# Kernel tuning notes

Measured on AMD Instinct MI355X. Metric: run time of the kernel, lower is better.

The kernel has to match this reference:

```python
import jax, jax.numpy as jnp
import numpy as np


def setup_inputs() -> dict:
    key = jax.random.key(0)
    ks = jax.random.split(key, 8)
    B, C, H, W = 4, 512, 64, 64
    Cq = C // 8
    s = 1.0 / np.sqrt(C)
    return {
        "x": jax.random.normal(ks[0], (B, C, H, W), jnp.float32),
        "Wq": jax.random.normal(ks[1], (Cq, C), jnp.float32) * s,
        "bq": jax.random.normal(ks[2], (Cq,), jnp.float32) * 0.01,
        "Wk": jax.random.normal(ks[3], (Cq, C), jnp.float32) * s,
        "bk": jax.random.normal(ks[4], (Cq,), jnp.float32) * 0.01,
        "Wv": jax.random.normal(ks[5], (C, C), jnp.float32) * s,
        "bv": jax.random.normal(ks[6], (C,), jnp.float32) * 0.01,
        "gamma": jax.random.normal(ks[7], (1,), jnp.float32),
    }


def reference(x, Wq, bq, Wk, bk, Wv, bv, gamma):
    B, C, H, W = x.shape
    N = H * W
    xf = x.reshape(B, C, N)  # flatten spatial; 1x1 conv == channel matmul
    q = jnp.einsum('oc,bcn->bon', Wq, xf) + bq[None, :, None]  # [B, C/8, N]
    k = jnp.einsum('oc,bcn->bon', Wk, xf) + bk[None, :, None]  # [B, C/8, N]
    v = jnp.einsum('oc,bcn->bon', Wv, xf) + bv[None, :, None]  # [B, C, N]
    energy = jnp.einsum('bdi,bdj->bij', q, k)                  # [B, N, N] (no scaling, as original)
    attention = jax.nn.softmax(energy, axis=-1)
    out = jnp.einsum('bcj,bij->bci', v, attention)             # bmm(v, att^T)
    out = out.reshape(B, C, H, W)
    return gamma[0] * out + x
```

## Files before the change

kernel.cpp:

```cpp
#include <hip/hip_runtime.h>


typedef float    f32x2 __attribute__((ext_vector_type(2)));
typedef float    f32x4 __attribute__((ext_vector_type(4)));
typedef _Float16 f16x4 __attribute__((ext_vector_type(4)));
typedef _Float16 f16x8 __attribute__((ext_vector_type(8)));
typedef short    bf16x8 __attribute__((ext_vector_type(8)));
typedef unsigned short u16x8 __attribute__((ext_vector_type(8)));

#define MFMA_F16(a, b, c)  __builtin_amdgcn_mfma_f32_16x16x32_f16((a), (b), (c), 0, 0, 0)
#define MFMA_BF16(a, b, c) __builtin_amdgcn_mfma_f32_16x16x32_bf16((a), (b), (c), 0, 0, 0)

__device__ __forceinline__ unsigned short bf16_rne(float f) {
    unsigned u = __builtin_bit_cast(unsigned, f);
    u += 0x7FFFu + ((u >> 16) & 1u);
    return (unsigned short)(u >> 16);
}
__device__ __forceinline__ float bf16_f(unsigned short h) {
    unsigned u = (unsigned)h << 16;
    return __builtin_bit_cast(float, u);
}

__device__ __forceinline__ void gload_lds16(const void* g, void* l) {
    __builtin_amdgcn_global_load_lds(
        (const __attribute__((address_space(1))) unsigned int*)g,
        (__attribute__((address_space(3))) unsigned int*)l, 16, 0, 0);
}

#define BARRIER_LGKM() do {                                   \
    asm volatile("s_waitcnt lgkmcnt(0)" ::: "memory");        \
    __builtin_amdgcn_s_barrier();                             \
    asm volatile("" ::: "memory");                            \
} while (0)

#define VM_WAIT8() do {                                       \
    asm volatile("s_waitcnt vmcnt(8)" ::: "memory");          \
    __builtin_amdgcn_sched_barrier(0);                        \
} while (0)
#define VM_WAIT0() do {                                       \
    asm volatile("s_waitcnt vmcnt(0)" ::: "memory");          \
    __builtin_amdgcn_sched_barrier(0);                        \
} while (0)

constexpr int BB = 4, CCH = 512, NS = 4096;

__global__ void prep_kernel(
    const float* __restrict__ Wq, const float* __restrict__ Wk,
    const float* __restrict__ Wv,
    _Float16* __restrict__ Wqh, _Float16* __restrict__ Wkh,
    _Float16* __restrict__ Wvh)
{
    const int idx = blockIdx.x * 256 + threadIdx.x;
    {
        f32x4 v = *(const f32x4*)&Wv[(size_t)idx * 4];
        f16x4 o;
#pragma unroll
        for (int e = 0; e < 4; ++e) o[e] = (_Float16)v[e];
        *(f16x4*)&Wvh[(size_t)idx * 4] = o;
    }
    if (idx < 8192) {
        f32x4 q = *(const f32x4*)&Wq[(size_t)idx * 4];
        f32x4 k = *(const f32x4*)&Wk[(size_t)idx * 4];
        f16x4 qo, ko;
#pragma unroll
        for (int e = 0; e < 4; ++e) { qo[e] = (_Float16)q[e]; ko[e] = (_Float16)k[e]; }
        *(f16x4*)&Wqh[(size_t)idx * 4] = qo;
        *(f16x4*)&Wkh[(size_t)idx * 4] = ko;
    }
}

__global__ __launch_bounds__(512, 4) void proj_kernel(
    const float* __restrict__ x,
    const _Float16* __restrict__ Wqh, const _Float16* __restrict__ Wkh,
    const _Float16* __restrict__ Wvh,
    const float* __restrict__ bq, const float* __restrict__ bk,
    const float* __restrict__ bv,
    _Float16* __restrict__ qws, _Float16* __restrict__ kws,
    unsigned short* __restrict__ vws)
{
    const int t = threadIdx.x, lane = t & 63, w = t >> 6;
    const int l15 = lane & 15, l4 = lane >> 4;
    const int b  = blockIdx.x >> 7;
    const int n0 = (blockIdx.x & 127) * 32;
    const float* xb = x + (size_t)b * CCH * NS;

    __shared__ _Float16 xt[2][32][64];

    f32x4 accv[4][2];
    f32x4 accq[2];
#pragma unroll
    for (int a = 0; a < 4; ++a)
#pragma unroll
        for (int n = 0; n < 2; ++n)
#pragma unroll
            for (int r = 0; r < 4; ++r) accv[a][n][r] = 0.f;
#pragma unroll
    for (int n = 0; n < 2; ++n)
#pragma unroll
        for (int r = 0; r < 4; ++r) accq[n][r] = 0.f;

    const _Float16* Wh = (w < 4) ? Wqh : Wkh;
    const int oq0 = (w & 3) * 16;
    const int stg_c = t >> 3;
    const int stg_n = (t & 7) * 4;

#define PROJ_STAGE(B) do {                                                     \
    char* xb_ = (char*)xt + (B) * 4096;                                        \
    _Pragma("unroll")                                                          \
    for (int u = 0; u < 4; ++u) {                                              \
        const int row = stg_n + u;                                             \
        const int g = ((stg_c >> 3) ^ (row & 7) ^ (((row >> 3) & 3) << 1)) & 7;\
        *(_Float16*)(xb_ + row * 128 + (g << 4) + (stg_c & 7) * 2)             \
            = (_Float16)xv[u];                                                 \
    }                                                                          \
} while (0)

    f32x4 xv = *(const f32x4*)&xb[(size_t)stg_c * NS + n0 + stg_n];
    PROJ_STAGE(0);
    xv = *(const f32x4*)&xb[(size_t)(64 + stg_c) * NS + n0 + stg_n];
    BARRIER_LGKM();

    for (int cc = 0; cc < 8; ++cc) {
        const int buf = cc & 1;
        f16x8 bh[2][2];
#pragma unroll
        for (int nf = 0; nf < 2; ++nf)
#pragma unroll
            for (int ds = 0; ds < 2; ++ds) {
                const int row = nf * 16 + l15;
                const int g = ((ds * 4 + l4) ^ (row & 7) ^ (((row >> 3) & 3) << 1)) & 7;
                bh[nf][ds] = *(const f16x8*)((char*)xt + buf * 4096 + row * 128 + (g << 4));
            }
        PROJ_STAGE(buf ^ 1);
        xv = *(const f32x4*)&xb[(size_t)((((cc + 2) & 7) * 64) + stg_c) * NS + n0 + stg_n];

#pragma unroll
        for (int ds = 0; ds < 2; ++ds) {
            const int c8 = cc * 64 + ds * 32 + l4 * 8;
            f16x8 ahq = *(const f16x8*)&Wh[(size_t)(oq0 + l15) * CCH + c8];
#pragma unroll
            for (int af = 0; af < 4; ++af) {
                f16x8 ah = *(const f16x8*)&Wvh[(size_t)(w * 64 + af * 16 + l15) * CCH + c8];
#pragma unroll
                for (int nf = 0; nf < 2; ++nf)
                    accv[af][nf] = MFMA_F16(ah, bh[nf][ds], accv[af][nf]);
            }
#pragma unroll
            for (int nf = 0; nf < 2; ++nf)
                accq[nf] = MFMA_F16(ahq, bh[nf][ds], accq[nf]);
        }
        BARRIER_LGKM();
    }
#undef PROJ_STAGE

#pragma unroll
    for (int af = 0; af < 4; ++af) {
#pragma unroll
        for (int r = 0; r < 4; ++r) {
            const int o = w * 64 + af * 16 + l4 * 4 + r;
            const float bias = bv[o];
#pragma unroll
            for (int nf = 0; nf < 2; ++nf) {
                const int n = n0 + nf * 16 + l15;
                vws[(size_t)(b * CCH + o) * NS + n] = bf16_rne(accv[af][nf][r] + bias);
            }
        }
    }
    {
        _Float16* oT = (w < 4) ? qws : kws;
        const float* bqk = (w < 4) ? bq : bk;
        float bias[4];
#pragma unroll
        for (int r = 0; r < 4; ++r) bias[r] = bqk[oq0 + l4 * 4 + r];
#pragma unroll
        for (int nf = 0; nf < 2; ++nf) {
            const int n = n0 + nf * 16 + l15;
            f16x4 hv;
#pragma unroll
            for (int r = 0; r < 4; ++r) hv[r] = (_Float16)(accq[nf][r] + bias[r]);
            *(f16x4*)&oT[((size_t)(b * NS + n)) * 64 + oq0 + l4 * 4] = hv;
        }
    }
}

__global__ __launch_bounds__(256, 4) void qk_kernel(
    const _Float16* __restrict__ qws, const _Float16* __restrict__ kws,
    unsigned short* __restrict__ Pws, float* __restrict__ lws2, int b0)
{
    const int t = threadIdx.x, lane = t & 63, w = t >> 6;
    const int l15 = lane & 15, l4 = lane >> 4;
    const int pb = blockIdx.x >> 8;
    const int b  = b0 + pb;
    const int r255 = blockIdx.x & 255;
    const int i0 = (r255 >> 1) * 32;
    const int jh = r255 & 1;
    const int jw = jh * 2048 + w * 512;

    __shared__ unsigned short Pt[4][32][32];
    __shared__ float Lred[4][32];

    f16x8 qa[2][2];
#pragma unroll
    for (int f = 0; f < 2; ++f)
#pragma unroll
        for (int ds = 0; ds < 2; ++ds)
            qa[f][ds] = *(const f16x8*)&qws[((size_t)(b * NS + i0 + f * 16 + l15)) * 64 + ds * 32 + l4 * 8];

    const _Float16* kb = kws + (size_t)b * NS * 64;
    f16x8 kf[2][2];
#pragma unroll
    for (int jf = 0; jf < 2; ++jf)
#pragma unroll
        for (int ds = 0; ds < 2; ++ds)
            kf[jf][ds] = *(const f16x8*)&kb[(size_t)(jw + jf * 16 + l15) * 64 + ds * 32 + l4 * 8];

    f32x4 lacc[2];
#pragma unroll
    for (int f = 0; f < 2; ++f)
#pragma unroll
        for (int r = 0; r < 4; ++r) lacc[f][r] = 0.f;

    char* wbase = (char*)&Pt[w][0][0];
    const int rrow = lane >> 1, h = lane & 1;
    const int rsw = (rrow & 3) ^ (((rrow >> 2) & 1) << 1);
    const int rg0 = (((2 * h)     ^ rsw) & 3) << 4;
    const int rg1 = (((2 * h + 1) ^ rsw) & 3) << 4;
    unsigned short* Pg = Pws + ((size_t)pb * NS + i0 + rrow) * NS + jw + h * 16;

    for (int jt = 0; jt < 16; ++jt) {
        f32x4 e[2][2];
#pragma unroll
        for (int f = 0; f < 2; ++f)
#pragma unroll
            for (int jf = 0; jf < 2; ++jf)
#pragma unroll
                for (int r = 0; r < 4; ++r) e[f][jf][r] = 0.f;
#pragma unroll
        for (int ds = 0; ds < 2; ++ds)
#pragma unroll
            for (int f = 0; f < 2; ++f)
#pragma unroll
                for (int jf = 0; jf < 2; ++jf)
                    e[f][jf] = MFMA_F16(qa[f][ds], kf[jf][ds], e[f][jf]);

        const int jn = jw + ((jt + 1) & 15) * 32;
#pragma unroll
        for (int jf = 0; jf < 2; ++jf)
#pragma unroll
            for (int ds = 0; ds < 2; ++ds)
                kf[jf][ds] = *(const f16x8*)&kb[(size_t)(jn + jf * 16 + l15) * 64 + ds * 32 + l4 * 8];

#pragma unroll
        for (int f = 0; f < 2; ++f)
#pragma unroll
            for (int jf = 0; jf < 2; ++jf) {
                const int col = jf * 16 + l15;
                const int cg = col >> 3;
#pragma unroll
                for (int r = 0; r < 4; ++r) {
                    const int row = f * 16 + l4 * 4 + r;
                    const unsigned short us = bf16_rne(__expf(e[f][jf][r]));
                    lacc[f][r] += bf16_f(us);
                    const int g = ((cg ^ (row & 3) ^ (((row >> 2) & 1) << 1)) & 3) << 4;
                    *(unsigned short*)(wbase + row * 64 + g + (col & 7) * 2) = us;
                }
            }

        asm volatile("s_waitcnt lgkmcnt(0)" ::: "memory");
        __builtin_amdgcn_sched_barrier(0);

        {
            u16x8 va = *(const u16x8*)(wbase + rrow * 64 + rg0);
            u16x8 vb = *(const u16x8*)(wbase + rrow * 64 + rg1);
            *(u16x8*)&Pg[jt * 32]     = va;
            *(u16x8*)&Pg[jt * 32 + 8] = vb;
        }
    }

#pragma unroll
    for (int f = 0; f < 2; ++f)
#pragma unroll
        for (int r = 0; r < 4; ++r) {
            float v = lacc[f][r];
            v += __shfl_xor(v, 1);
            v += __shfl_xor(v, 2);
            v += __shfl_xor(v, 4);
            v += __shfl_xor(v, 8);
            if (l15 == 0) Lred[w][f * 16 + l4 * 4 + r] = v;
        }
    __syncthreads();
    if (t < 32) {
        const float s = Lred[0][t] + Lred[1][t] + Lred[2][t] + Lred[3][t];
        lws2[((size_t)jh * BB + b) * NS + i0 + t] = s;
    }
}

__global__ __launch_bounds__(256, 2) void pv_kernel(
    const unsigned short* __restrict__ Pws, const unsigned short* __restrict__ vws,
    const float* __restrict__ lws2, const float* __restrict__ x,
    const float* __restrict__ gamma, float* __restrict__ out, int b0, int cpx)
{
    const int t = threadIdx.x, lane = t & 63, w = t >> 6;
    const int l15 = lane & 15, l4 = lane >> 4;
    const int bid = (int)blockIdx.x;
    const int swzid = (bid & 7) * cpx + (bid >> 3);
    const int pb = swzid >> 7;
    const int b  = b0 + pb;
    const int r7 = swzid & 127;
    const int in = r7 >> 2, cm = r7 & 3;
    const int wr = w >> 1, wc = w & 1;

    __shared__ unsigned short Vt[2][128][64];
    __shared__ unsigned short Pt2[2][128][64];

    const int srow = w * 8 + (lane >> 3);
    const int sg   = (lane & 7) ^ (srow & 7);
    const unsigned short* gV = vws + ((size_t)(b * CCH + cm * 128 + srow)) * NS + sg * 8;
    const unsigned short* gP = Pws + ((size_t)(pb * NS + in * 128 + srow)) * NS + sg * 8;

    f32x4 acc[4][4];
#pragma unroll
    for (int m = 0; m < 4; ++m)
#pragma unroll
        for (int n = 0; n < 4; ++n)
#pragma unroll
            for (int r = 0; r < 4; ++r) acc[m][n][r] = 0.f;

    int offa[2][4], offb[2][4];
#pragma unroll
    for (int kk = 0; kk < 2; ++kk) {
        const int g = (kk * 4 + l4) ^ (l15 & 7);
#pragma unroll
        for (int m = 0; m < 4; ++m) {
            offa[kk][m] = (wr * 64 + m * 16 + l15) * 128 + g * 16;
            offb[kk][m] = (wc * 64 + m * 16 + l15) * 128 + g * 16;
        }
    }

#define PV_STAGE(kt, buf) do {                                                  \
    const unsigned short* _gV = gV + (size_t)(kt) * 64;                         \
    const unsigned short* _gP = gP + (size_t)(kt) * 64;                         \
    char* _lV = (char*)&Vt[buf][0][0]  + w * 1024;                              \
    char* _lP = (char*)&Pt2[buf][0][0] + w * 1024;                              \
    _Pragma("unroll")                                                           \
    for (int q = 0; q < 4; ++q) {                                               \
        gload_lds16(_gV + (size_t)q * 32 * NS, _lV + q * 4096);                 \
        gload_lds16(_gP + (size_t)q * 32 * NS, _lP + q * 4096);                 \
    }                                                                           \
} while (0)

#define PV_COMPUTE(buf) do {                                                    \
    __builtin_amdgcn_s_setprio(1);                                              \
    _Pragma("unroll")                                                           \
    for (int kk = 0; kk < 2; ++kk) {                                            \
        bf16x8 a[4], bfr[4];                                                    \
        _Pragma("unroll")                                                       \
        for (int m = 0; m < 4; ++m) {                                           \
            a[m]   = *(const bf16x8*)((char*)&Vt[buf][0][0]  + offa[kk][m]);    \
            bfr[m] = *(const bf16x8*)((char*)&Pt2[buf][0][0] + offb[kk][m]);    \
        }                                                                       \
        _Pragma("unroll")                                                       \
        for (int m = 0; m < 4; ++m)                                             \
            _Pragma("unroll")                                                   \
            for (int n = 0; n < 4; ++n)                                         \
                acc[m][n] = MFMA_BF16(a[m], bfr[n], acc[m][n]);                 \
    }                                                                           \
    __builtin_amdgcn_s_setprio(0);                                              \
} while (0)

    PV_STAGE(0, 0);
    for (int kt = 0; kt < 62; kt += 2) {
        PV_STAGE(kt + 1, 1);
        VM_WAIT8();
        __builtin_amdgcn_s_barrier();
        PV_COMPUTE(0);
        BARRIER_LGKM();
        PV_STAGE(kt + 2, 0);
        VM_WAIT8();
        __builtin_amdgcn_s_barrier();
        PV_COMPUTE(1);
        BARRIER_LGKM();
    }
    PV_STAGE(63, 1);
    VM_WAIT8();
    __builtin_amdgcn_s_barrier();
    PV_COMPUTE(0);
    BARRIER_LGKM();
    VM_WAIT0();
    __builtin_amdgcn_s_barrier();
    PV_COMPUTE(1);

#undef PV_STAGE
#undef PV_COMPUTE

    const float gm = gamma[0];
    float linv[4];
#pragma unroll
    for (int n = 0; n < 4; ++n) {
        const int i = in * 128 + wc * 64 + n * 16 + l15;
        linv[n] = 1.f / (lws2[(size_t)b * NS + i] +
                         lws2[((size_t)BB + b) * NS + i]);
    }
#pragma unroll
    for (int m = 0; m < 4; ++m) {
#pragma unroll
        for (int r = 0; r < 4; ++r) {
            const int c = cm * 128 + wr * 64 + m * 16 + l4 * 4 + r;
            const float* xr = x + ((size_t)(b * CCH + c)) * NS;
            float* orow = out + ((size_t)(b * CCH + c)) * NS;
#pragma unroll
            for (int n = 0; n < 4; ++n) {
                const int i = in * 128 + wc * 64 + n * 16 + l15;
                orow[i] = gm * acc[m][n][r] * linv[n] + xr[i];
            }
        }
    }
}

extern "C" void kernel_launch(void* const* d_in, const int* in_sizes, int n_in,
                              void* d_out, int out_size, void* d_ws, size_t ws_size,
                              hipStream_t stream)
{
    const float* x     = (const float*)d_in[0];
    const float* Wq    = (const float*)d_in[1];
    const float* bq    = (const float*)d_in[2];
    const float* Wk    = (const float*)d_in[3];
    const float* bk    = (const float*)d_in[4];
    const float* Wv    = (const float*)d_in[5];
    const float* bv    = (const float*)d_in[6];
    const float* gamma = (const float*)d_in[7];
    float* out = (float*)d_out;

    char* p = (char*)d_ws;
    size_t off = 0;
    auto take = [&](size_t bytes) { char* r = p + off; off += (bytes + 255) & ~(size_t)255; return r; };
    _Float16* qws       = (_Float16*)take((size_t)BB * NS * 64 * 2);
    _Float16* kws       = (_Float16*)take((size_t)BB * NS * 64 * 2);
    unsigned short* vws = (unsigned short*)take((size_t)BB * CCH * NS * 2);
    _Float16* Wvh       = (_Float16*)take((size_t)CCH * CCH * 2);
    _Float16* Wqh       = (_Float16*)take((size_t)64 * CCH * 2);
    _Float16* Wkh       = (_Float16*)take((size_t)64 * CCH * 2);
    float* lws2         = (float*)take((size_t)2 * BB * NS * 4);
    unsigned short* Pws = (unsigned short*)(p + off);

    const size_t P_PER_B = (size_t)NS * NS * 2;
    size_t avail = (ws_size > off) ? (ws_size - off) : 0;
    int nb = (int)(avail / P_PER_B);
    if (nb >= 4) nb = 4; else if (nb >= 2) nb = 2; else nb = 1;

    prep_kernel<<<256, 256, 0, stream>>>(Wq, Wk, Wv, Wqh, Wkh, Wvh);
    proj_kernel<<<512, 512, 0, stream>>>(x, Wqh, Wkh, Wvh, bq, bk, bv,
                                         qws, kws, vws);
    for (int b0 = 0; b0 < BB; b0 += nb) {
        const int nbb = (b0 + nb <= BB) ? nb : (BB - b0);
        qk_kernel<<<nbb * 256, 256, 0, stream>>>(qws, kws, Pws, lws2, b0);
        pv_kernel<<<nbb * 128, 256, 0, stream>>>(Pws, vws, lws2, x, gamma, out,
                                                 b0, (nbb * 128) >> 3);
    }
}
```

Baseline: 167.9 us.

## Enlarge PV tile to 128x256 per block with 8-column MFMA fragments per wave

The PV kernel's output tile grows from 128 channels x 128 positions to 128 x 256 positions. Each wave now holds a 4x8 accumulator array, and the grid shrinks from 128 to 64 blocks per batch. The P staging buffer doubles and the load pattern and vmcnt wait are adjusted to match. This is meant to raise arithmetic intensity and cut redundant V loads from HBM. The cost is more registers, with launch bounds lowered to one block per SIMD, and fewer blocks (256 total) to spread across the CUs.

```diff
diff --git a/kernel.cpp b/kernel.cpp
--- a/kernel.cpp
+++ b/kernel.cpp
@@ -33,8 +33,8 @@
     asm volatile("" ::: "memory");                            \
 } while (0)
 
-#define VM_WAIT8() do {                                       \
-    asm volatile("s_waitcnt vmcnt(8)" ::: "memory");          \
+#define VM_WAIT12() do {                                      \
+    asm volatile("s_waitcnt vmcnt(12)" ::: "memory");         \
     __builtin_amdgcn_sched_barrier(0);                        \
 } while (0)
 #define VM_WAIT0() do {                                       \
@@ -295,7 +295,7 @@
     }
 }
 
-__global__ __launch_bounds__(256, 2) void pv_kernel(
+__global__ __launch_bounds__(256, 1) void pv_kernel(
     const unsigned short* __restrict__ Pws, const unsigned short* __restrict__ vws,
     const float* __restrict__ lws2, const float* __restrict__ x,
     const float* __restrict__ gamma, float* __restrict__ out, int b0, int cpx)
@@ -304,66 +304,69 @@
     const int l15 = lane & 15, l4 = lane >> 4;
     const int bid = (int)blockIdx.x;
     const int swzid = (bid & 7) * cpx + (bid >> 3);
-    const int pb = swzid >> 7;
+    const int pb = swzid >> 6;
     const int b  = b0 + pb;
-    const int r7 = swzid & 127;
-    const int in = r7 >> 2, cm = r7 & 3;
+    const int r6 = swzid & 63;
+    const int in = r6 >> 2, cm = r6 & 3;
     const int wr = w >> 1, wc = w & 1;
 
     __shared__ unsigned short Vt[2][128][64];
-    __shared__ unsigned short Pt2[2][128][64];
-
-    const int srow = w * 8 + (lane >> 3);
-    const int sg   = (lane & 7) ^ (srow & 7);
-    const unsigned short* gV = vws + ((size_t)(b * CCH + cm * 128 + srow)) * NS + sg * 8;
-    const unsigned short* gP = Pws + ((size_t)(pb * NS + in * 128 + srow)) * NS + sg * 8;
-
-    f32x4 acc[4][4];
+    __shared__ unsigned short Pt2[2][256][64];
+
+    const int lrow = lane >> 3;
+    const int sg   = (lane & 7) ^ lrow;
+    const unsigned short* gV = vws + ((size_t)(b * CCH + cm * 128 + w * 32 + lrow)) * NS + sg * 8;
+    const unsigned short* gP = Pws + ((size_t)pb * NS + in * 256 + w * 64 + lrow) * NS + sg * 8;
+
+    f32x4 acc[4][8];
 #pragma unroll
     for (int m = 0; m < 4; ++m)
 #pragma unroll
-        for (int n = 0; n < 4; ++n)
+        for (int n = 0; n < 8; ++n)
 #pragma unroll
             for (int r = 0; r < 4; ++r) acc[m][n][r] = 0.f;
 
-    int offa[2][4], offb[2][4];
+    int offa[2][4], offb[2][8];
 #pragma unroll
     for (int kk = 0; kk < 2; ++kk) {
         const int g = (kk * 4 + l4) ^ (l15 & 7);
 #pragma unroll
-        for (int m = 0; m < 4; ++m) {
+        for (int m = 0; m < 4; ++m)
             offa[kk][m] = (wr * 64 + m * 16 + l15) * 128 + g * 16;
-            offb[kk][m] = (wc * 64 + m * 16 + l15) * 128 + g * 16;
-        }
+#pragma unroll
+        for (int n = 0; n < 8; ++n)
+            offb[kk][n] = (wc * 128 + n * 16 + l15) * 128 + g * 16;
     }
 
 #define PV_STAGE(kt, buf) do {                                                  \
     const unsigned short* _gV = gV + (size_t)(kt) * 64;                         \
     const unsigned short* _gP = gP + (size_t)(kt) * 64;                         \
-    char* _lV = (char*)&Vt[buf][0][0]  + w * 1024;                              \
-    char* _lP = (char*)&Pt2[buf][0][0] + w * 1024;                              \
+    char* _lV = (char*)&Vt[buf][0][0]  + w * 4096;       \
+    char* _lP = (char*)&Pt2[buf][0][0] + w * 8192;       \
     _Pragma("unroll")                                                           \
-    for (int q = 0; q < 4; ++q) {                                               \
-        gload_lds16(_gV + (size_t)q * 32 * NS, _lV + q * 4096);                 \
-        gload_lds16(_gP + (size_t)q * 32 * NS, _lP + q * 4096);                 \
-    }                                                                           \
+    for (int q = 0; q < 4; ++q)                                                 \
+        gload_lds16(_gV + (size_t)q * 8 * NS, _lV + q * 1024);                  \
+    _Pragma("unroll")                                                           \
+    for (int q = 0; q < 8; ++q)                                                 \
+        gload_lds16(_gP + (size_t)q * 8 * NS, _lP + q * 1024);                  \
 } while (0)
 
 #define PV_COMPUTE(buf) do {                                                    \
     __builtin_amdgcn_s_setprio(1);                                              \
     _Pragma("unroll")                                                           \
     for (int kk = 0; kk < 2; ++kk) {                                            \
-        bf16x8 a[4], bfr[4];                                                    \
+        bf16x8 a[4], bb[8];                                                     \
         _Pragma("unroll")                                                       \
-        for (int m = 0; m < 4; ++m) {                                           \
-            a[m]   = *(const bf16x8*)((char*)&Vt[buf][0][0]  + offa[kk][m]);    \
-            bfr[m] = *(const bf16x8*)((char*)&Pt2[buf][0][0] + offb[kk][m]);    \
-        }                                                                       \
+        for (int m = 0; m < 4; ++m)                                             \
+            a[m] = *(const bf16x8*)((char*)&Vt[buf][0][0] + offa[kk][m]);       \
+        _Pragma("unroll")                                                       \
+        for (int n = 0; n < 8; ++n)                                             \
+            bb[n] = *(const bf16x8*)((char*)&Pt2[buf][0][0] + offb[kk][n]);     \
         _Pragma("unroll")                                                       \
         for (int m = 0; m < 4; ++m)                                             \
             _Pragma("unroll")                                                   \
-            for (int n = 0; n < 4; ++n)                                         \
-                acc[m][n] = MFMA_BF16(a[m], bfr[n], acc[m][n]);                 \
+            for (int n = 0; n < 8; ++n)                                         \
+                acc[m][n] = MFMA_BF16(a[m], bb[n], acc[m][n]);                  \
     }                                                                           \
     __builtin_amdgcn_s_setprio(0);                                              \
 } while (0)
@@ -371,18 +374,18 @@
     PV_STAGE(0, 0);
     for (int kt = 0; kt < 62; kt += 2) {
         PV_STAGE(kt + 1, 1);
-        VM_WAIT8();
+        VM_WAIT12();
         __builtin_amdgcn_s_barrier();
         PV_COMPUTE(0);
         BARRIER_LGKM();
         PV_STAGE(kt + 2, 0);
-        VM_WAIT8();
+        VM_WAIT12();
         __builtin_amdgcn_s_barrier();
         PV_COMPUTE(1);
         BARRIER_LGKM();
     }
     PV_STAGE(63, 1);
-    VM_WAIT8();
+    VM_WAIT12();
     __builtin_amdgcn_s_barrier();
     PV_COMPUTE(0);
     BARRIER_LGKM();
@@ -394,10 +397,10 @@
 #undef PV_COMPUTE
 
     const float gm = gamma[0];
-    float linv[4];
-#pragma unroll
-    for (int n = 0; n < 4; ++n) {
-        const int i = in * 128 + wc * 64 + n * 16 + l15;
+    float linv[8];
+#pragma unroll
+    for (int n = 0; n < 8; ++n) {
+        const int i = in * 256 + wc * 128 + n * 16 + l15;
         linv[n] = 1.f / (lws2[(size_t)b * NS + i] +
                          lws2[((size_t)BB + b) * NS + i]);
     }
@@ -409,8 +412,8 @@
             const float* xr = x + ((size_t)(b * CCH + c)) * NS;
             float* orow = out + ((size_t)(b * CCH + c)) * NS;
 #pragma unroll
-            for (int n = 0; n < 4; ++n) {
-                const int i = in * 128 + wc * 64 + n * 16 + l15;
+            for (int n = 0; n < 8; ++n) {
+                const int i = in * 256 + wc * 128 + n * 16 + l15;
                 orow[i] = gm * acc[m][n][r] * linv[n] + xr[i];
             }
         }
@@ -454,7 +457,7 @@
     for (int b0 = 0; b0 < BB; b0 += nb) {
         const int nbb = (b0 + nb <= BB) ? nb : (BB - b0);
         qk_kernel<<<nbb * 256, 256, 0, stream>>>(qws, kws, Pws, lws2, b0);
-        pv_kernel<<<nbb * 128, 256, 0, stream>>>(Pws, vws, lws2, x, gamma, out,
-                                                 b0, (nbb * 128) >> 3);
-    }
-}
+        pv_kernel<<<nbb * 64, 256, 0, stream>>>(Pws, vws, lws2, x, gamma, out,
+                                                b0, (nbb * 64) >> 3);
+    }
+}
```

Result: slower. 197.6 us (+17.7%).
